# Optimization experiments

Hardware: AMD Instinct MI355X
Metric: run time of the kernel (lower is better)

Reference implementation:

```python
import jax, jax.numpy as jnp
import numpy as np

IN_DIM = 256
AT_DIM = 256
NUM_HEAD = 4
COMPRESS_QK = 8
D_QK = (AT_DIM // NUM_HEAD) // COMPRESS_QK  # 8, per-head qkv channels
AT_HEAD = AT_DIM // NUM_HEAD               # 64, per-head output channels
B, H, W = 2, 64, 64


def setup_inputs() -> dict:
    key = jax.random.key(0)
    ks = jax.random.split(key, 11)
    s = 0.02
    x = jax.random.normal(ks[0], (B, IN_DIM, H, W), dtype=jnp.float32)
    Wq = jax.random.normal(ks[1], (NUM_HEAD, D_QK, IN_DIM), dtype=jnp.float32) * s
    bq = jax.random.normal(ks[2], (NUM_HEAD, D_QK), dtype=jnp.float32) * s
    Wk = jax.random.normal(ks[3], (NUM_HEAD, D_QK, IN_DIM), dtype=jnp.float32) * s
    bk = jax.random.normal(ks[4], (NUM_HEAD, D_QK), dtype=jnp.float32) * s
    Wv = jax.random.normal(ks[5], (NUM_HEAD, D_QK, IN_DIM), dtype=jnp.float32) * s
    bv = jax.random.normal(ks[6], (NUM_HEAD, D_QK), dtype=jnp.float32) * s
    Wo = jax.random.normal(ks[7], (NUM_HEAD, AT_HEAD, D_QK), dtype=jnp.float32) * s
    bo = jax.random.normal(ks[8], (NUM_HEAD, AT_HEAD), dtype=jnp.float32) * s
    gamma = jax.random.normal(ks[9], (NUM_HEAD,), dtype=jnp.float32)  # torch inits 0; random for nontrivial test
    return {"x": x, "Wq": Wq, "bq": bq, "Wk": Wk, "bk": bk, "Wv": Wv,
            "bv": bv, "Wo": Wo, "bo": bo, "gamma": gamma}


def reference(x, Wq, bq, Wk, bk, Wv, bv, Wo, bo, gamma):
    b, C, h, w = x.shape
    N = h * w
    xf = x.reshape(b, C, N)  # flatten spatial -> [b, C, N]
    # 1x1 convs as channel contractions, all heads batched: [b, nh, d, N]
    q = jnp.einsum('hdc,bcn->bhdn', Wq, xf) + bq[None, :, :, None]
    k = jnp.einsum('hdc,bcn->bhdn', Wk, xf) + bk[None, :, :, None]
    v = jnp.einsum('hdc,bcn->bhdn', Wv, xf) + bv[None, :, :, None]
    # S[n,m] = sum_d q[d,n] * k[d,m]  (proj_query^T @ proj_key)
    S = jnp.einsum('bhdn,bhdm->bhnm', q, k)
    # torch softmax(dim=-2): normalize over rows n for each column m
    A = jax.nn.softmax(S, axis=-2)
    # proj_value @ attention_map_T : [b,h,d,m]
    o = jnp.einsum('bhdn,bhnm->bhdm', v, A)
    # out_conv 1x1: d -> AT_HEAD, then gamma scale
    y = jnp.einsum('hed,bhdm->bhem', Wo, o) + bo[None, :, :, None]
    y = gamma[None, :, None, None] * y
    # concat heads along channel dim, add residual
    out = y.reshape(b, NUM_HEAD * AT_HEAD, h, w) + x
    return out
```

## Files before the change

### kernel.cpp

```cpp
#include <hip/hip_runtime.h>
#include <hip/hip_bf16.h>

#define IN_DIM 256
#define NH 4
#define DQK 8
#define ATH 64
#define NB 2
#define NSP 4096
#define LOG2E 1.44269504088896f

typedef __attribute__((ext_vector_type(8))) short short8;
typedef __attribute__((ext_vector_type(16))) float f32x16;

#define Q_OFF 0u
#define K_OFF (512u * 1024u)
#define VR_OFF (1024u * 1024u)
#define VF_OFF (1536u * 1024u)
#define P_OFF (3584u * 1024u)

__device__ __forceinline__ float fast_exp2(float x) {
#if __has_builtin(__builtin_amdgcn_exp2f)
    return __builtin_amdgcn_exp2f(x);
#else
    return exp2f(x);
#endif
}

__device__ __forceinline__ unsigned bf_rne(float f) {
    unsigned u = __float_as_uint(f);
    u += 0x7FFFu + ((u >> 16) & 1u);
    return u >> 16;
}
__device__ __forceinline__ unsigned pack2bf(float a, float b) {
    return bf_rne(a) | (bf_rne(b) << 16);
}
__device__ __forceinline__ unsigned pack2bf_tr(float a, float b) {
    return (__float_as_uint(a) >> 16) | (__float_as_uint(b) & 0xFFFF0000u);
}

__global__ __launch_bounds__(64) void qkv_gemm(
    const float* __restrict__ x,
    const float* __restrict__ Wq, const float* __restrict__ bq,
    const float* __restrict__ Wk, const float* __restrict__ bk,
    const float* __restrict__ Wv, const float* __restrict__ bv,
    unsigned char* __restrict__ ws)
{
    const int lane = threadIdx.x;
    const int nt = blockIdx.x;
    const int mt = blockIdx.y;
    const int b  = blockIdx.z;
    const int col = lane & 31;
    const int hp  = lane >> 5;

    const int R = mt * 32 + col;
    const int h = R / 24;
    const int r24 = R % 24;
    const int sel = r24 >> 3;
    const int dd = r24 & 7;
    const float* Wsel = (sel == 0) ? Wq : (sel == 1) ? Wk : Wv;
    const float* wrow = Wsel + (h * DQK + dd) * IN_DIM;

    const float* xb = x + (size_t)b * IN_DIM * NSP + (size_t)(hp * 8) * NSP + nt * 32 + col;

    union U4 { uint4 u; short8 s; };
    f32x16 acc = {};

#pragma unroll
    for (int kt = 0; kt < 16; ++kt) {
        const float4 wa = *(const float4*)(wrow + kt * 16 + hp * 8);
        const float4 wb = *(const float4*)(wrow + kt * 16 + hp * 8 + 4);
        U4 af;
        af.u.x = pack2bf(wa.x, wa.y);
        af.u.y = pack2bf(wa.z, wa.w);
        af.u.z = pack2bf(wb.x, wb.y);
        af.u.w = pack2bf(wb.z, wb.w);

        float xv[8];
#pragma unroll
        for (int j = 0; j < 8; ++j) xv[j] = xb[(size_t)(kt * 16 + j) * NSP];
        U4 bfm;
        bfm.u.x = pack2bf(xv[0], xv[1]);
        bfm.u.y = pack2bf(xv[2], xv[3]);
        bfm.u.z = pack2bf(xv[4], xv[5]);
        bfm.u.w = pack2bf(xv[6], xv[7]);

        acc = __builtin_amdgcn_mfma_f32_32x32x16_bf16(af.s, bfm.s, acc, 0, 0, 0);
    }

    const int n = nt * 32 + col;
#pragma unroll
    for (int p = 0; p < 2; ++p) {
        const int gA = 2 * p, gB = 2 * p + 1;
        const int RA = mt * 32 + 8 * gA, RB = mt * 32 + 8 * gB;
        const int hA = RA / 24, hB = RB / 24;
        const int selA = (RA % 24) >> 3, selB = (RB % 24) >> 3;
        const float* bsA = (selA == 0) ? bq : (selA == 1) ? bk : bv;
        const float* bsB = (selB == 0) ? bq : (selB == 1) ? bk : bv;
        const float scA = (selA == 1) ? LOG2E : 1.0f;
        const float scB = (selB == 1) ? LOG2E : 1.0f;

        float vA[4], vB[4];
#pragma unroll
        for (int j = 0; j < 4; ++j) {
            vA[j] = (acc[4 * gA + j] + bsA[hA * DQK + 4 * hp + j]) * scA;
            vB[j] = (acc[4 * gB + j] + bsB[hB * DQK + 4 * hp + j]) * scB;
        }
        const unsigned PA0 = pack2bf(vA[0], vA[1]), PA1 = pack2bf(vA[2], vA[3]);
        const unsigned PB0 = pack2bf(vB[0], vB[1]), PB1 = pack2bf(vB[2], vB[3]);

        const int s0 = hp ? (int)PA0 : (int)PB0;
        const int s1 = hp ? (int)PA1 : (int)PB1;
        const unsigned r0 = (unsigned)__shfl_xor(s0, 32, 64);
        const unsigned r1 = (unsigned)__shfl_xor(s1, 32, 64);

        const uint4 row = hp ? make_uint4(r0, r1, PB0, PB1)
                             : make_uint4(PA0, PA1, r0, r1);

        const unsigned offA = (selA == 0) ? Q_OFF : (selA == 1) ? K_OFF : VR_OFF;
        const unsigned offB = (selB == 0) ? Q_OFF : (selB == 1) ? K_OFF : VR_OFF;
        unsigned char* dA = ws + offA + ((size_t)(b * NH + hA) * NSP + n) * 16;
        unsigned char* dB = ws + offB + ((size_t)(b * NH + hB) * NSP + n) * 16;
        *(uint4*)(hp ? dB : dA) = row;
    }
}

__global__ __launch_bounds__(64) void vfrag_kernel(unsigned char* __restrict__ ws)
{
    const int tid = threadIdx.x;
    if (tid >= 36) return;
    const int T = blockIdx.x;
    const int bh = blockIdx.y;
    const int e = tid % 9;
    const int r = tid / 9;
    const int h2 = r & 1, c2 = r >> 1;

    unsigned char* dst = ws + VF_OFF + (size_t)bh * 262144u +
                         (size_t)((T * 2 + c2) * 64 + 32 * h2 + e) * 16;
    if (e == 8) {
        *(uint4*)dst = make_uint4(0x3F803F80u, 0x3F803F80u, 0x3F803F80u, 0x3F803F80u);
        return;
    }
    const unsigned char* src = ws + VR_OFF +
        ((size_t)bh * NSP + T * 32 + c2 * 16 + h2 * 8) * 16 + e * 2;
    unsigned w0 = 0, w1 = 0, w2 = 0, w3 = 0;
    w0 = (unsigned)*(const unsigned short*)(src + 0 * 16) |
         ((unsigned)*(const unsigned short*)(src + 1 * 16) << 16);
    w1 = (unsigned)*(const unsigned short*)(src + 2 * 16) |
         ((unsigned)*(const unsigned short*)(src + 3 * 16) << 16);
    w2 = (unsigned)*(const unsigned short*)(src + 4 * 16) |
         ((unsigned)*(const unsigned short*)(src + 5 * 16) << 16);
    w3 = (unsigned)*(const unsigned short*)(src + 6 * 16) |
         ((unsigned)*(const unsigned short*)(src + 7 * 16) << 16);
    *(uint4*)dst = make_uint4(w0, w1, w2, w3);
}

__global__ __launch_bounds__(64, 4) void attn_partial(unsigned char* __restrict__ ws)
{
    const int lane = threadIdx.x;
    const int mt = blockIdx.x;
    const int bh = blockIdx.y;
    const int nq = blockIdx.z;
    const int e = lane & 31;
    const int hp = lane >> 5;

    union U4 { uint4 u; short8 s; };
    const uint4 zero4 = make_uint4(0, 0, 0, 0);

    U4 kf;
    kf.u = (hp == 0)
        ? *(const uint4*)(ws + K_OFF + ((size_t)bh * NSP + mt * 32 + e) * 16)
        : zero4;

    const uint4* qrows = (const uint4*)(ws + Q_OFF + (size_t)bh * NSP * 16);
    const uint4* vfr = (const uint4*)(ws + VF_OFF + (size_t)bh * 262144u);

    f32x16 acc = {};
    const f32x16 zc = {};

    const int nt0 = nq * 32;
    U4 qf_n, vf0_n, vf1_n;
    qf_n.u = (hp == 0) ? qrows[nt0 * 32 + e] : zero4;
    vf0_n.u = vfr[(nt0 * 2 + 0) * 64 + lane];
    vf1_n.u = vfr[(nt0 * 2 + 1) * 64 + lane];

    for (int t = 0; t < 32; ++t) {
        U4 qf = qf_n, vf0 = vf0_n, vf1 = vf1_n;
        if (t < 31) {
            const int nt = nt0 + t + 1;
            qf_n.u = (hp == 0) ? qrows[nt * 32 + e] : zero4;
            vf0_n.u = vfr[(nt * 2 + 0) * 64 + lane];
            vf1_n.u = vfr[(nt * 2 + 1) * 64 + lane];
        }

        f32x16 S = __builtin_amdgcn_mfma_f32_32x32x16_bf16(qf.s, kf.s, zc, 0, 0, 0);

        unsigned Qd[8];
#pragma unroll
        for (int i = 0; i < 8; ++i) {
            const float a = fast_exp2(S[2 * i]);
            const float b2 = fast_exp2(S[2 * i + 1]);
            Qd[i] = pack2bf_tr(a, b2);
        }

        const int sA0 = hp ? Qd[0] : Qd[2];
        const int sA1 = hp ? Qd[1] : Qd[3];
        const int rA0 = __shfl_xor(sA0, 32, 64);
        const int rA1 = __shfl_xor(sA1, 32, 64);
        const int sB0 = hp ? Qd[4] : Qd[6];
        const int sB1 = hp ? Qd[5] : Qd[7];
        const int rB0 = __shfl_xor(sB0, 32, 64);
        const int rB1 = __shfl_xor(sB1, 32, 64);

        U4 f0, f1;
        f0.u = hp ? make_uint4(rA0, rA1, Qd[2], Qd[3])
                  : make_uint4(Qd[0], Qd[1], rA0, rA1);
        f1.u = hp ? make_uint4(rB0, rB1, Qd[6], Qd[7])
                  : make_uint4(Qd[4], Qd[5], rB0, rB1);

        acc = __builtin_amdgcn_mfma_f32_32x32x16_bf16(f0.s, vf0.s, acc, 0, 0, 0);
        acc = __builtin_amdgcn_mfma_f32_32x32x16_bf16(f1.s, vf1.s, acc, 0, 0, 0);
    }

    if (e <= 8) {
        float* pp = (float*)(ws + P_OFF) +
                    ((((size_t)bh * 128 + mt) * 4 + nq) * 18 + hp * 9 + e) * 16;
#pragma unroll
        for (int r = 0; r < 16; ++r) pp[r] = acc[r];
    }
}

__global__ __launch_bounds__(256) void attn_epilogue(
    const unsigned char* __restrict__ ws,
    const float* __restrict__ x,
    const float* __restrict__ Wo, const float* __restrict__ bo,
    const float* __restrict__ gamma,
    float* __restrict__ out)
{
    __shared__ float sO[128 * 13];
    const int tid = threadIdx.x;
    const int ms = blockIdx.x;
    const int bh = blockIdx.y;
    const int h = bh & (NH - 1);
    const int b = bh >> 2;

    const float* P = (const float*)(ws + P_OFF);
    for (int idx = tid; idx < 128 * 9; idx += 256) {
        const int m_l = idx / 9, e = idx % 9;
        const int mt = ms * 4 + (m_l >> 5);
        const int m32 = m_l & 31;
        const int hp = (m32 >> 2) & 1;
        const int r = (m32 & 3) + 4 * (m32 >> 3);
        const size_t base = ((((size_t)bh * 128 + mt) * 4) * 18 + hp * 9 + e) * 16 + r;
        const float s = P[base] + P[base + 18 * 16] +
                        P[base + 2 * 18 * 16] + P[base + 3 * 18 * 16];
        sO[m_l * 13 + e] = s;
    }
    __syncthreads();

    const int m_l = tid & 127;
    const int half = tid >> 7;
    const float rl = 1.0f / sO[m_l * 13 + 8];
    float od[DQK];
#pragma unroll
    for (int d = 0; d < DQK; ++d) od[d] = sO[m_l * 13 + d] * rl;

    const float g = gamma[h];
    const int mg = ms * 128 + m_l;
#pragma unroll
    for (int eo = half * 32; eo < half * 32 + 32; ++eo) {
        const float* wo = Wo + (h * ATH + eo) * DQK;
        float y = bo[h * ATH + eo];
#pragma unroll
        for (int d = 0; d < DQK; ++d) y = fmaf(wo[d], od[d], y);
        const size_t oi = ((size_t)(b * IN_DIM) + h * ATH + eo) * NSP + mg;
        out[oi] = fmaf(g, y, x[oi]);
    }
}

extern "C" void kernel_launch(void* const* d_in, const int* in_sizes, int n_in,
                              void* d_out, int out_size, void* d_ws, size_t ws_size,
                              hipStream_t stream)
{
    const float* x = (const float*)d_in[0];
    const float* Wq = (const float*)d_in[1];
    const float* bq = (const float*)d_in[2];
    const float* Wk = (const float*)d_in[3];
    const float* bk = (const float*)d_in[4];
    const float* Wv = (const float*)d_in[5];
    const float* bv = (const float*)d_in[6];
    const float* Wo = (const float*)d_in[7];
    const float* bo = (const float*)d_in[8];
    const float* gamma = (const float*)d_in[9];
    float* out = (float*)d_out;
    unsigned char* ws = (unsigned char*)d_ws;

    qkv_gemm<<<dim3(128, 3, NB), 64, 0, stream>>>(
        x, Wq, bq, Wk, bk, Wv, bv, ws);
    vfrag_kernel<<<dim3(128, NB * NH), 64, 0, stream>>>(ws);
    attn_partial<<<dim3(128, NB * NH, 4), 64, 0, stream>>>(ws);
    attn_epilogue<<<dim3(32, NB * NH), 256, 0, stream>>>(
        ws, x, Wo, bo, gamma, out);
}
```

Before: 119.9 us.

## Fuse V-fragment packing into QKV GEMM and epilogue into attention via last-block counter

The QKV GEMM now writes V directly in the MFMA fragment layout, which removes the separate vfrag kernel and the raw V buffer. The attention partial and epilogue kernels are merged: each block writes its partial sums, bumps an atomic counter, and the last of the four split-N blocks reduces the partials and applies the output projection, gamma and residual. Counters are zeroed inside the GEMM kernel, and a byte-permute intrinsic is used for bf16 truncation packing. This cuts two kernel launches and a round trip, at the cost of scattered 2-byte stores, thread fences, and an epilogue that runs with only 64 threads per tile.

Result: slower. 262.3 us (+118.7%).

```diff
diff --git a/kernel.cpp b/kernel.cpp
--- a/kernel.cpp
+++ b/kernel.cpp
@@ -14,9 +14,9 @@
 
 #define Q_OFF 0u
 #define K_OFF (512u * 1024u)
-#define VR_OFF (1024u * 1024u)
-#define VF_OFF (1536u * 1024u)
-#define P_OFF (3584u * 1024u)
+#define VF_OFF (1024u * 1024u)
+#define P_OFF (3u * 1024u * 1024u)
+#define C_OFF (8u * 1024u * 1024u)
 
 __device__ __forceinline__ float fast_exp2(float x) {
 #if __has_builtin(__builtin_amdgcn_exp2f)
@@ -35,7 +35,11 @@
     return bf_rne(a) | (bf_rne(b) << 16);
 }
 __device__ __forceinline__ unsigned pack2bf_tr(float a, float b) {
+#if __has_builtin(__builtin_amdgcn_perm)
+    return __builtin_amdgcn_perm(__float_as_uint(b), __float_as_uint(a), 0x07060302u);
+#else
     return (__float_as_uint(a) >> 16) | (__float_as_uint(b) & 0xFFFF0000u);
+#endif
 }
 
 __global__ __launch_bounds__(64) void qkv_gemm(
@@ -52,6 +56,12 @@
     const int col = lane & 31;
     const int hp  = lane >> 5;
 
+    if (nt == 0 && mt == 0 && b == 0) {
+        int* cnt = (int*)(ws + C_OFF);
+#pragma unroll
+        for (int i = 0; i < 16; ++i) cnt[i * 64 + lane] = 0;
+    }
+
     const int R = mt * 32 + col;
     const int h = R / 24;
     const int r24 = R % 24;
@@ -116,45 +126,37 @@
         const uint4 row = hp ? make_uint4(r0, r1, PB0, PB1)
                              : make_uint4(PA0, PA1, r0, r1);
 
-        const unsigned offA = (selA == 0) ? Q_OFF : (selA == 1) ? K_OFF : VR_OFF;
-        const unsigned offB = (selB == 0) ? Q_OFF : (selB == 1) ? K_OFF : VR_OFF;
-        unsigned char* dA = ws + offA + ((size_t)(b * NH + hA) * NSP + n) * 16;
-        unsigned char* dB = ws + offB + ((size_t)(b * NH + hB) * NSP + n) * 16;
-        *(uint4*)(hp ? dB : dA) = row;
-    }
-}
-
-__global__ __launch_bounds__(64) void vfrag_kernel(unsigned char* __restrict__ ws)
-{
-    const int tid = threadIdx.x;
-    if (tid >= 36) return;
-    const int T = blockIdx.x;
-    const int bh = blockIdx.y;
-    const int e = tid % 9;
-    const int r = tid / 9;
-    const int h2 = r & 1, c2 = r >> 1;
-
-    unsigned char* dst = ws + VF_OFF + (size_t)bh * 262144u +
-                         (size_t)((T * 2 + c2) * 64 + 32 * h2 + e) * 16;
-    if (e == 8) {
-        *(uint4*)dst = make_uint4(0x3F803F80u, 0x3F803F80u, 0x3F803F80u, 0x3F803F80u);
-        return;
-    }
-    const unsigned char* src = ws + VR_OFF +
-        ((size_t)bh * NSP + T * 32 + c2 * 16 + h2 * 8) * 16 + e * 2;
-    unsigned w0 = 0, w1 = 0, w2 = 0, w3 = 0;
-    w0 = (unsigned)*(const unsigned short*)(src + 0 * 16) |
-         ((unsigned)*(const unsigned short*)(src + 1 * 16) << 16);
-    w1 = (unsigned)*(const unsigned short*)(src + 2 * 16) |
-         ((unsigned)*(const unsigned short*)(src + 3 * 16) << 16);
-    w2 = (unsigned)*(const unsigned short*)(src + 4 * 16) |
-         ((unsigned)*(const unsigned short*)(src + 5 * 16) << 16);
-    w3 = (unsigned)*(const unsigned short*)(src + 6 * 16) |
-         ((unsigned)*(const unsigned short*)(src + 7 * 16) << 16);
-    *(uint4*)dst = make_uint4(w0, w1, w2, w3);
-}
-
-__global__ __launch_bounds__(64, 4) void attn_partial(unsigned char* __restrict__ ws)
+        const int selX = hp ? selB : selA;
+        const int hX = hp ? hB : hA;
+        const int bhX = b * NH + hX;
+
+        if (selX == 2) {
+            unsigned char* dst = ws + VF_OFF + (size_t)bhX * 262144u +
+                (size_t)((nt * 2 + ((col >> 4) & 1)) * 64 + 32 * ((col >> 3) & 1)) * 16 +
+                (col & 7) * 2;
+            *(unsigned short*)(dst + 0 * 16) = (unsigned short)(row.x);
+            *(unsigned short*)(dst + 1 * 16) = (unsigned short)(row.x >> 16);
+            *(unsigned short*)(dst + 2 * 16) = (unsigned short)(row.y);
+            *(unsigned short*)(dst + 3 * 16) = (unsigned short)(row.y >> 16);
+            *(unsigned short*)(dst + 4 * 16) = (unsigned short)(row.z);
+            *(unsigned short*)(dst + 5 * 16) = (unsigned short)(row.z >> 16);
+            *(unsigned short*)(dst + 6 * 16) = (unsigned short)(row.w);
+            *(unsigned short*)(dst + 7 * 16) = (unsigned short)(row.w >> 16);
+            *(unsigned short*)(dst + 8 * 16) = 0x3F80;
+        } else {
+            unsigned char* d = ws + ((selX == 0) ? Q_OFF : K_OFF) +
+                               ((size_t)bhX * NSP + n) * 16;
+            *(uint4*)d = row;
+        }
+    }
+}
+
+__global__ __launch_bounds__(64, 4) void attn_fused(
+    unsigned char* __restrict__ ws,
+    const float* __restrict__ x,
+    const float* __restrict__ Wo, const float* __restrict__ bo,
+    const float* __restrict__ gamma,
+    float* __restrict__ out)
 {
     const int lane = threadIdx.x;
     const int mt = blockIdx.x;
@@ -221,53 +223,48 @@
         acc = __builtin_amdgcn_mfma_f32_32x32x16_bf16(f1.s, vf1.s, acc, 0, 0, 0);
     }
 
+    float* P = (float*)(ws + P_OFF);
     if (e <= 8) {
-        float* pp = (float*)(ws + P_OFF) +
-                    ((((size_t)bh * 128 + mt) * 4 + nq) * 18 + hp * 9 + e) * 16;
-#pragma unroll
-        for (int r = 0; r < 16; ++r) pp[r] = acc[r];
-    }
-}
-
-__global__ __launch_bounds__(256) void attn_epilogue(
-    const unsigned char* __restrict__ ws,
-    const float* __restrict__ x,
-    const float* __restrict__ Wo, const float* __restrict__ bo,
-    const float* __restrict__ gamma,
-    float* __restrict__ out)
-{
-    __shared__ float sO[128 * 13];
-    const int tid = threadIdx.x;
-    const int ms = blockIdx.x;
-    const int bh = blockIdx.y;
+        float* pp = P + ((((size_t)bh * 128 + mt) * 4 + nq) * 18 + hp * 9 + e) * 16;
+        *(float4*)(pp + 0)  = make_float4(acc[0], acc[1], acc[2], acc[3]);
+        *(float4*)(pp + 4)  = make_float4(acc[4], acc[5], acc[6], acc[7]);
+        *(float4*)(pp + 8)  = make_float4(acc[8], acc[9], acc[10], acc[11]);
+        *(float4*)(pp + 12) = make_float4(acc[12], acc[13], acc[14], acc[15]);
+    }
+
+    __threadfence();
+    __shared__ int s_old;
+    if (lane == 0) {
+        int* cnt = (int*)(ws + C_OFF) + bh * 128 + mt;
+        s_old = atomicAdd(cnt, 1);
+    }
+    __syncthreads();
+    if (s_old != 3) return;
+    __threadfence();
+
+    __shared__ float sO[32 * 9];
+    const float* Pb = P + ((size_t)bh * 128 + mt) * 4 * 288;
+    for (int idx = lane; idx < 288; idx += 64) {
+        const int slot = idx >> 4, r = idx & 15;
+        const int hp2 = slot / 9, e2 = slot - hp2 * 9;
+        const int m = (r & 3) + 8 * (r >> 2) + 4 * hp2;
+        sO[m * 9 + e2] = Pb[idx] + Pb[288 + idx] + Pb[576 + idx] + Pb[864 + idx];
+    }
+    __syncthreads();
+
     const int h = bh & (NH - 1);
     const int b = bh >> 2;
-
-    const float* P = (const float*)(ws + P_OFF);
-    for (int idx = tid; idx < 128 * 9; idx += 256) {
-        const int m_l = idx / 9, e = idx % 9;
-        const int mt = ms * 4 + (m_l >> 5);
-        const int m32 = m_l & 31;
-        const int hp = (m32 >> 2) & 1;
-        const int r = (m32 & 3) + 4 * (m32 >> 3);
-        const size_t base = ((((size_t)bh * 128 + mt) * 4) * 18 + hp * 9 + e) * 16 + r;
-        const float s = P[base] + P[base + 18 * 16] +
-                        P[base + 2 * 18 * 16] + P[base + 3 * 18 * 16];
-        sO[m_l * 13 + e] = s;
-    }
-    __syncthreads();
-
-    const int m_l = tid & 127;
-    const int half = tid >> 7;
-    const float rl = 1.0f / sO[m_l * 13 + 8];
+    const int m = lane & 31;
+    const float rl = 1.0f / sO[m * 9 + 8];
     float od[DQK];
 #pragma unroll
-    for (int d = 0; d < DQK; ++d) od[d] = sO[m_l * 13 + d] * rl;
+    for (int d = 0; d < DQK; ++d) od[d] = sO[m * 9 + d] * rl;
 
     const float g = gamma[h];
-    const int mg = ms * 128 + m_l;
-#pragma unroll
-    for (int eo = half * 32; eo < half * 32 + 32; ++eo) {
+    const int mg = mt * 32 + m;
+#pragma unroll 8
+    for (int i = 0; i < 32; ++i) {
+        const int eo = hp * 32 + i;
         const float* wo = Wo + (h * ATH + eo) * DQK;
         float y = bo[h * ATH + eo];
 #pragma unroll
@@ -296,8 +293,6 @@
 
     qkv_gemm<<<dim3(128, 3, NB), 64, 0, stream>>>(
         x, Wq, bq, Wk, bk, Wv, bv, ws);
-    vfrag_kernel<<<dim3(128, NB * NH), 64, 0, stream>>>(ws);
-    attn_partial<<<dim3(128, NB * NH, 4), 64, 0, stream>>>(ws);
-    attn_epilogue<<<dim3(32, NB * NH), 256, 0, stream>>>(
+    attn_fused<<<dim3(128, NB * NH, 4), 64, 0, stream>>>(
         ws, x, Wo, bo, gamma, out);
 }
```
